# Kernel optimization log

Hardware: AMD Instinct MI355X
Metric: run time of the kernel (lower is better)

Reference implementation:

```python
import jax, jax.numpy as jnp
import numpy as np

N = 8192      # nodes
F = 256       # in_features
H = 64        # hidden_dim
NEG = -9e15   # mask fill value from the torch source
EPS = 1e-5    # LayerNorm eps (torch default)


def setup_inputs() -> dict:
    key = jax.random.key(0)
    ks = jax.random.split(key, 6)
    x = jax.random.normal(ks[0], (N, F), jnp.float32)
    adj = jax.random.randint(ks[1], (N, N), 0, 2, jnp.int32)
    # Linear params (xavier-ish scale, zero bias as in reset_parameters)
    Wt = jax.random.normal(ks[2], (H, F), jnp.float32) * (1.0 / np.sqrt(F))
    bt = jnp.zeros((H,), jnp.float32)
    Wa = jax.random.normal(ks[3], (1, H), jnp.float32) * (1.0 / np.sqrt(H))
    ba = jnp.zeros((1,), jnp.float32)
    Wp = jax.random.normal(ks[4], (F, H), jnp.float32) * (1.0 / np.sqrt(H))
    bp = jnp.zeros((F,), jnp.float32)
    gamma = jnp.ones((F,), jnp.float32)
    beta = jnp.zeros((F,), jnp.float32)
    return dict(x=x, adj=adj, Wt=Wt, bt=bt, Wa=Wa, ba=ba,
                Wp=Wp, bp=bp, gamma=gamma, beta=beta)


def reference(x, adj, Wt, bt, Wa, ba, Wp, bp, gamma, beta):
    # h = feature_transform(x): [N, H]
    h = x @ Wt.T + bt
    # per-source-node scalar score, expanded over all N columns: [N, 1]
    s = jax.nn.leaky_relu(h @ Wa.T + ba, negative_slope=0.2)
    # adjacency-masked softmax over neighbors (dim=1); s broadcasts to [N, N]
    scores = jnp.where(adj > 0, s, jnp.float32(NEG))
    w = jax.nn.softmax(scores, axis=1)            # [N, N]
    # dropout inactive at inference -> identity
    neighbor = w @ h                               # [N, H]
    tf = neighbor @ Wp.T + bp                      # [N, F]
    # residual + LayerNorm
    y = x + tf
    mu = jnp.mean(y, axis=-1, keepdims=True)
    var = jnp.var(y, axis=-1, keepdims=True)
    return gamma * (y - mu) * jax.lax.rsqrt(var + EPS) + beta
```

## Files before the change

### kernel.cpp

```cpp
#include <hip/hip_runtime.h>
#include <stdint.h>

#define NN 8192
#define FF 256
#define HH 64

typedef __attribute__((ext_vector_type(8))) short bf16x8;
typedef __attribute__((ext_vector_type(4))) float f32x4;

__device__ __forceinline__ uint16_t f2bf(float f) {
  union { float f; uint32_t i; } c; c.f = f;
  uint32_t r = c.i + 0x7FFFu + ((c.i >> 16) & 1u);
  return (uint16_t)(r >> 16);
}

__global__ __launch_bounds__(256) void k1_h(
    const float* __restrict__ x, const float* __restrict__ Wt,
    const float* __restrict__ bt, uint16_t* __restrict__ hT) {
  __shared__ float wtT[256 * 65];
  __shared__ float sbt[64];
  __shared__ uint16_t s_tr[64][34];
  const int t = threadIdx.x;
  const int lane = t & 63;
  const int w = t >> 6;

  for (int i = 0; i < 64; ++i)
    wtT[t * 65 + i] = Wt[(size_t)i * FF + t];
  if (t < 64) sbt[t] = bt[t];
  __syncthreads();

  const int n0 = blockIdx.x * 32;
  const int r0 = n0 + w * 8;
  const float binit = sbt[lane];
  float acc[8];
#pragma unroll
  for (int r = 0; r < 8; ++r) acc[r] = binit;

  for (int f4 = 0; f4 < FF; f4 += 4) {
    float4 xs[8];
#pragma unroll
    for (int r = 0; r < 8; ++r)
      xs[r] = *(const float4*)(x + (size_t)(r0 + r) * FF + f4);
    const float wt0 = wtT[(f4 + 0) * 65 + lane];
    const float wt1 = wtT[(f4 + 1) * 65 + lane];
    const float wt2 = wtT[(f4 + 2) * 65 + lane];
    const float wt3 = wtT[(f4 + 3) * 65 + lane];
#pragma unroll
    for (int r = 0; r < 8; ++r)
      acc[r] += xs[r].x * wt0 + xs[r].y * wt1 + xs[r].z * wt2 + xs[r].w * wt3;
  }

#pragma unroll
  for (int r = 0; r < 8; ++r)
    s_tr[lane][w * 8 + r] = f2bf(acc[r]);
  __syncthreads();
#pragma unroll
  for (int i = 0; i < 4; ++i) {
    int idx = i * 256 + t;
    int c = idx >> 4;
    int d = idx & 15;
    uint32_t v = (uint32_t)s_tr[c][2 * d] | ((uint32_t)s_tr[c][2 * d + 1] << 16);
    *(uint32_t*)(hT + (size_t)c * NN + n0 + 2 * d) = v;
  }
}

__global__ __launch_bounds__(256) void k2f(
    const int* __restrict__ adj, const uint16_t* __restrict__ hT,
    const float* __restrict__ x, const float* __restrict__ Wp,
    const float* __restrict__ bp, const float* __restrict__ gamma,
    const float* __restrict__ beta, float* __restrict__ out) {
  __shared__ __align__(16) unsigned char smem[49408];
  unsigned char* af = smem;
  float (*s_part)[16][64] = (float (*)[16][64])(smem + 32768);
  float (*s_degw)[16]     = (float (*)[16])(smem + 32768 + 16384);
  float (*s_nb)[64]       = (float (*)[64])(smem);
  float* s_y              = (float*)(smem + 4096);

  const int t    = threadIdx.x;
  const int w    = t >> 6;
  const int lane = t & 63;
  const int m    = lane & 15;
  const int q    = lane >> 4;
  const int row0 = blockIdx.x * 16;

  bf16x8 vone;
#pragma unroll
  for (int j = 0; j < 8; ++j) vone[j] = (short)0x3F80;

  f32x4 acc0 = 0, acc1 = 0, acc2 = 0, acc3 = 0, accd = 0;
  const uint16_t* __restrict__ hrow = hT + (size_t)m * NN;
  const int rsw = (m & 7) << 4;

  for (int tile = 0; tile < 8; ++tile) {
    const int c0 = tile * 1024;
#pragma unroll
    for (int i = 0; i < 16; ++i) {
      int4 a = *(const int4*)(adj + (size_t)(row0 + i) * NN + c0 + t * 4);
      uint32_t lo = ((uint32_t)a.x | ((uint32_t)a.y << 16)) * 0x3F80u;
      uint32_t hi = ((uint32_t)a.z | ((uint32_t)a.w << 16)) * 0x3F80u;
      uint2 w2; w2.x = lo; w2.y = hi;
      uint32_t boff = (uint32_t)(t * 8) ^ (uint32_t)((i & 7) << 4);
      *(uint2*)(af + (i << 11) + boff) = w2;
    }
    __syncthreads();
#pragma unroll
    for (int it = 0; it < 4; ++it) {
      const int kl = w * 256 + it * 64;
      const int k0 = c0 + kl + q * 8;
      const int k1 = k0 + 32;
      bf16x8 afA = *(const bf16x8*)(af + (m << 11) +
                                    ((uint32_t)((kl + q * 8) * 2) ^ rsw));
      bf16x8 afB = *(const bf16x8*)(af + (m << 11) +
                                    ((uint32_t)((kl + q * 8 + 32) * 2) ^ rsw));
      bf16x8 b0 = *(const bf16x8*)(hrow + k0);
      bf16x8 b1 = *(const bf16x8*)(hrow + 16 * NN + k0);
      bf16x8 b2 = *(const bf16x8*)(hrow + 32 * NN + k0);
      bf16x8 b3 = *(const bf16x8*)(hrow + 48 * NN + k0);
      bf16x8 d0 = *(const bf16x8*)(hrow + k1);
      bf16x8 d1 = *(const bf16x8*)(hrow + 16 * NN + k1);
      bf16x8 d2 = *(const bf16x8*)(hrow + 32 * NN + k1);
      bf16x8 d3 = *(const bf16x8*)(hrow + 48 * NN + k1);
      acc0 = __builtin_amdgcn_mfma_f32_16x16x32_bf16(afA, b0, acc0, 0, 0, 0);
      acc1 = __builtin_amdgcn_mfma_f32_16x16x32_bf16(afA, b1, acc1, 0, 0, 0);
      acc2 = __builtin_amdgcn_mfma_f32_16x16x32_bf16(afA, b2, acc2, 0, 0, 0);
      acc3 = __builtin_amdgcn_mfma_f32_16x16x32_bf16(afA, b3, acc3, 0, 0, 0);
      accd = __builtin_amdgcn_mfma_f32_16x16x32_bf16(afA, vone, accd, 0, 0, 0);
      acc0 = __builtin_amdgcn_mfma_f32_16x16x32_bf16(afB, d0, acc0, 0, 0, 0);
      acc1 = __builtin_amdgcn_mfma_f32_16x16x32_bf16(afB, d1, acc1, 0, 0, 0);
      acc2 = __builtin_amdgcn_mfma_f32_16x16x32_bf16(afB, d2, acc2, 0, 0, 0);
      acc3 = __builtin_amdgcn_mfma_f32_16x16x32_bf16(afB, d3, acc3, 0, 0, 0);
      accd = __builtin_amdgcn_mfma_f32_16x16x32_bf16(afB, vone, accd, 0, 0, 0);
    }
    __syncthreads();
  }

#pragma unroll
  for (int rg = 0; rg < 4; ++rg) {
    (*s_part)[0][0] = (*s_part)[0][0];
  }
#pragma unroll
  for (int rg = 0; rg < 4; ++rg) {
    s_part[w][q * 4 + rg][ 0 + m] = acc0[rg];
    s_part[w][q * 4 + rg][16 + m] = acc1[rg];
    s_part[w][q * 4 + rg][32 + m] = acc2[rg];
    s_part[w][q * 4 + rg][48 + m] = acc3[rg];
  }
  if (m == 0) {
#pragma unroll
    for (int rg = 0; rg < 4; ++rg) s_degw[w][q * 4 + rg] = accd[rg];
  }
  __syncthreads();

  for (int idx = t; idx < 16 * 64; idx += 256) {
    int r = idx >> 6, c = idx & 63;
    float s = s_part[0][r][c] + s_part[1][r][c] +
              s_part[2][r][c] + s_part[3][r][c];
    float d = s_degw[0][r] + s_degw[1][r] + s_degw[2][r] + s_degw[3][r];
    s_nb[r][c] = (d > 0.5f) ? s / d : 0.f;
  }
  __syncthreads();

  {
    const int f = t;
    float wp[64];
    const float* wrow = Wp + (size_t)f * HH;
#pragma unroll
    for (int j = 0; j < 16; ++j) {
      float4 v = *(const float4*)(wrow + j * 4);
      wp[j * 4 + 0] = v.x; wp[j * 4 + 1] = v.y;
      wp[j * 4 + 2] = v.z; wp[j * 4 + 3] = v.w;
    }
    const float bpf = bp[f];
    for (int r = 0; r < 16; ++r) {
      float a = bpf;
#pragma unroll
      for (int k = 0; k < 64; k += 4) {
        float4 nv = *(const float4*)&s_nb[r][k];
        a += nv.x * wp[k] + nv.y * wp[k + 1] + nv.z * wp[k + 2] + nv.w * wp[k + 3];
      }
      float y = x[(size_t)(row0 + r) * FF + f] + a;
      s_y[r * 256 + f] = y;
    }
  }
  __syncthreads();

  for (int i = 0; i < 4; ++i) {
    const int r = w * 4 + i;
    float4 v = *(const float4*)&s_y[r * 256 + lane * 4];
    float sum = v.x + v.y + v.z + v.w;
    float ss  = v.x * v.x + v.y * v.y + v.z * v.z + v.w * v.w;
#pragma unroll
    for (int o = 32; o >= 1; o >>= 1) {
      sum += __shfl_xor(sum, o, 64);
      ss  += __shfl_xor(ss, o, 64);
    }
    const float mu  = sum * (1.0f / 256.0f);
    const float var = ss * (1.0f / 256.0f) - mu * mu;
    const float rs  = rsqrtf(var + 1e-5f);
    const int f0 = lane * 4;
    float4 g = *(const float4*)(gamma + f0);
    float4 b = *(const float4*)(beta + f0);
    float4 o4;
    o4.x = g.x * (v.x - mu) * rs + b.x;
    o4.y = g.y * (v.y - mu) * rs + b.y;
    o4.z = g.z * (v.z - mu) * rs + b.z;
    o4.w = g.w * (v.w - mu) * rs + b.w;
    *(float4*)(out + (size_t)(row0 + r) * FF + f0) = o4;
  }
}

extern "C" void kernel_launch(void* const* d_in, const int* in_sizes, int n_in,
                              void* d_out, int out_size, void* d_ws, size_t ws_size,
                              hipStream_t stream) {
  const float* x     = (const float*)d_in[0];
  const int*   adj   = (const int*)d_in[1];
  const float* Wt    = (const float*)d_in[2];
  const float* bt    = (const float*)d_in[3];
  const float* Wp    = (const float*)d_in[6];
  const float* bp    = (const float*)d_in[7];
  const float* gamma = (const float*)d_in[8];
  const float* beta  = (const float*)d_in[9];
  float* out = (float*)d_out;

  uint16_t* hT = (uint16_t*)d_ws;

  k1_h<<<256, 256, 0, stream>>>(x, Wt, bt, hT);
  k2f <<<512, 256, 0, stream>>>(adj, hT, x, Wp, bp, gamma, beta, out);
}
```

Baseline: 476.5 us.

## Split neighbor aggregation across two column halves and move epilogue to separate kernel

The fused attention kernel is split so each 16-row group is handled by two blocks, each covering half of the adjacency columns. This doubles the grid to 1024 blocks for better occupancy across CUs. Each block writes partial neighbor sums and degrees to workspace, and a new epilogue kernel combines the halves and does the projection, residual and LayerNorm. The cost is an extra kernel launch plus a round trip of the partials through global memory.

```diff
diff --git a/kernel.cpp b/kernel.cpp
--- a/kernel.cpp
+++ b/kernel.cpp
@@ -64,24 +64,22 @@
   }
 }
 
-__global__ __launch_bounds__(256) void k2f(
+__global__ __launch_bounds__(256) void k2_attn(
     const int* __restrict__ adj, const uint16_t* __restrict__ hT,
-    const float* __restrict__ x, const float* __restrict__ Wp,
-    const float* __restrict__ bp, const float* __restrict__ gamma,
-    const float* __restrict__ beta, float* __restrict__ out) {
-  __shared__ __align__(16) unsigned char smem[49408];
-  unsigned char* af = smem;
-  float (*s_part)[16][64] = (float (*)[16][64])(smem + 32768);
-  float (*s_degw)[16]     = (float (*)[16])(smem + 32768 + 16384);
-  float (*s_nb)[64]       = (float (*)[64])(smem);
-  float* s_y              = (float*)(smem + 4096);
+    float* __restrict__ nb_part, float* __restrict__ deg_part) {
+  __shared__ __align__(16) unsigned char af[16 * 1024];
+  __shared__ float s_part[4][16][64];
+  __shared__ float s_degw[4][16];
 
   const int t    = threadIdx.x;
   const int w    = t >> 6;
   const int lane = t & 63;
   const int m    = lane & 15;
   const int q    = lane >> 4;
-  const int row0 = blockIdx.x * 16;
+  const int g    = blockIdx.x >> 1;
+  const int half = blockIdx.x & 1;
+  const int row0 = g * 16;
+  const int rsw  = (m & 7) << 4;
 
   bf16x8 vone;
 #pragma unroll
@@ -89,29 +87,31 @@
 
   f32x4 acc0 = 0, acc1 = 0, acc2 = 0, acc3 = 0, accd = 0;
   const uint16_t* __restrict__ hrow = hT + (size_t)m * NN;
-  const int rsw = (m & 7) << 4;
-
+  const int sr = t >> 7;
+  const int sc = t & 127;
+
+  const int base = half * (NN / 2);
   for (int tile = 0; tile < 8; ++tile) {
-    const int c0 = tile * 1024;
-#pragma unroll
-    for (int i = 0; i < 16; ++i) {
-      int4 a = *(const int4*)(adj + (size_t)(row0 + i) * NN + c0 + t * 4);
+    const int c0 = base + tile * 512;
+#pragma unroll
+    for (int i = 0; i < 8; ++i) {
+      const int r_ = 2 * i + sr;
+      int4 a = *(const int4*)(adj + (size_t)(row0 + r_) * NN + c0 + sc * 4);
       uint32_t lo = ((uint32_t)a.x | ((uint32_t)a.y << 16)) * 0x3F80u;
       uint32_t hi = ((uint32_t)a.z | ((uint32_t)a.w << 16)) * 0x3F80u;
       uint2 w2; w2.x = lo; w2.y = hi;
-      uint32_t boff = (uint32_t)(t * 8) ^ (uint32_t)((i & 7) << 4);
-      *(uint2*)(af + (i << 11) + boff) = w2;
+      *(uint2*)(af + r_ * 1024 + (((uint32_t)(sc * 8)) ^ ((r_ & 7) << 4))) = w2;
     }
     __syncthreads();
 #pragma unroll
-    for (int it = 0; it < 4; ++it) {
-      const int kl = w * 256 + it * 64;
+    for (int it = 0; it < 2; ++it) {
+      const int kl = w * 128 + it * 64;
       const int k0 = c0 + kl + q * 8;
       const int k1 = k0 + 32;
-      bf16x8 afA = *(const bf16x8*)(af + (m << 11) +
-                                    ((uint32_t)((kl + q * 8) * 2) ^ rsw));
-      bf16x8 afB = *(const bf16x8*)(af + (m << 11) +
-                                    ((uint32_t)((kl + q * 8 + 32) * 2) ^ rsw));
+      bf16x8 afA = *(const bf16x8*)(af + m * 1024 +
+                                    (((uint32_t)((kl + q * 8) * 2)) ^ rsw));
+      bf16x8 afB = *(const bf16x8*)(af + m * 1024 +
+                                    (((uint32_t)((kl + q * 8) * 2 + 64)) ^ rsw));
       bf16x8 b0 = *(const bf16x8*)(hrow + k0);
       bf16x8 b1 = *(const bf16x8*)(hrow + 16 * NN + k0);
       bf16x8 b2 = *(const bf16x8*)(hrow + 32 * NN + k0);
@@ -136,10 +136,6 @@
 
 #pragma unroll
   for (int rg = 0; rg < 4; ++rg) {
-    (*s_part)[0][0] = (*s_part)[0][0];
-  }
-#pragma unroll
-  for (int rg = 0; rg < 4; ++rg) {
     s_part[w][q * 4 + rg][ 0 + m] = acc0[rg];
     s_part[w][q * 4 + rg][16 + m] = acc1[rg];
     s_part[w][q * 4 + rg][32 + m] = acc2[rg];
@@ -151,11 +147,37 @@
   }
   __syncthreads();
 
+  float* __restrict__ dst = nb_part + ((size_t)half * NN + row0) * HH;
   for (int idx = t; idx < 16 * 64; idx += 256) {
     int r = idx >> 6, c = idx & 63;
     float s = s_part[0][r][c] + s_part[1][r][c] +
               s_part[2][r][c] + s_part[3][r][c];
-    float d = s_degw[0][r] + s_degw[1][r] + s_degw[2][r] + s_degw[3][r];
+    dst[(size_t)r * HH + c] = s;
+  }
+  if (t < 16) {
+    float d = s_degw[0][t] + s_degw[1][t] + s_degw[2][t] + s_degw[3][t];
+    deg_part[half * NN + row0 + t] = d;
+  }
+}
+
+__global__ __launch_bounds__(256) void k3_epi(
+    const float* __restrict__ x, const float* __restrict__ nb_part,
+    const float* __restrict__ deg_part, const float* __restrict__ Wp,
+    const float* __restrict__ bp, const float* __restrict__ gamma,
+    const float* __restrict__ beta, float* __restrict__ out) {
+  __shared__ float s_nb[16][64];
+  __shared__ float s_y[16 * 256];
+
+  const int t    = threadIdx.x;
+  const int w    = t >> 6;
+  const int lane = t & 63;
+  const int row0 = blockIdx.x * 16;
+
+  for (int idx = t; idx < 16 * 64; idx += 256) {
+    int r = idx >> 6, c = idx & 63;
+    float d = deg_part[row0 + r] + deg_part[NN + row0 + r];
+    float s = nb_part[(size_t)(row0 + r) * HH + c] +
+              nb_part[(size_t)(NN + row0 + r) * HH + c];
     s_nb[r][c] = (d > 0.5f) ? s / d : 0.f;
   }
   __syncthreads();
@@ -222,8 +244,11 @@
   const float* beta  = (const float*)d_in[9];
   float* out = (float*)d_out;
 
-  uint16_t* hT = (uint16_t*)d_ws;
-
-  k1_h<<<256, 256, 0, stream>>>(x, Wt, bt, hT);
-  k2f <<<512, 256, 0, stream>>>(adj, hT, x, Wp, bp, gamma, beta, out);
-}
+  uint16_t* hT       = (uint16_t*)d_ws;
+  float*    nb_part  = (float*)((char*)d_ws + (1u << 20));
+  float*    deg_part = (float*)((char*)d_ws + (5u << 20));
+
+  k1_h   <<<256,  256, 0, stream>>>(x, Wt, bt, hT);
+  k2_attn<<<1024, 256, 0, stream>>>(adj, hT, nb_part, deg_part);
+  k3_epi <<<512,  256, 0, stream>>>(x, nb_part, deg_part, Wp, bp, gamma, beta, out);
+}
```

After: 436.7 us. 8.4% less time.
